# Kernel optimization log

Hardware: AMD Instinct MI355X
Metric: run time of the kernel (lower is better)

Reference implementation:

```python
import jax, jax.numpy as jnp
import numpy as np

EPS = 1e-5  # torch InstanceNorm2d default eps


def _pe_2d(h, w, dim):
    """2D rotary angles: first dim//2 channel-pairs encode row position, rest encode col.
    Returns angles of shape (dim//2, h, w) -- one angle per channel PAIR."""
    half = dim // 2          # channels per axis
    nf = half // 2           # rotation pairs per axis
    inv = 1.0 / (10000.0 ** (jnp.arange(nf, dtype=jnp.float32) * 2.0 / half))
    ang_h = jnp.arange(h, dtype=jnp.float32)[None, :, None] * inv[:, None, None]  # (nf,h,1)
    ang_w = jnp.arange(w, dtype=jnp.float32)[None, None, :] * inv[:, None, None]  # (nf,1,w)
    ang_h = jnp.broadcast_to(ang_h, (nf, h, w))
    ang_w = jnp.broadcast_to(ang_w, (nf, h, w))
    return jnp.concatenate([ang_h, ang_w], axis=0)  # (dim//2, h, w)


def _rope_2d(x, ang):
    """Rotate consecutive channel pairs (2i, 2i+1) of x [b,c,h,w] by angles [c//2,h,w]."""
    b, c, h, w = x.shape
    x1 = x[:, 0::2]  # (b, c//2, h, w)
    x2 = x[:, 1::2]
    cos = jnp.cos(ang)[None]
    sin = jnp.sin(ang)[None]
    r1 = x1 * cos - x2 * sin
    r2 = x1 * sin + x2 * cos
    return jnp.stack([r1, r2], axis=2).reshape(b, c, h, w)


def _conv1x1(t, W, b):
    return jnp.einsum('bchw,oc->bohw', t, W) + b[None, :, None, None]


def setup_inputs() -> dict:
    key = jax.random.key(0)
    ks = jax.random.split(key, 11)
    B, C, H, W, S, O = 16, 256, 64, 64, 128, 256
    f = lambda k, sh: jax.random.normal(k, sh, dtype=jnp.float32)
    return {
        'x': f(ks[0], (B, C, H, W)),
        'gate_W': f(ks[1], (C, C)) * 0.05,  'gate_b': f(ks[2], (C,)) * 0.05,
        'value_W': f(ks[3], (C, C)) * 0.05, 'value_b': f(ks[4], (C,)) * 0.05,
        'z_W': f(ks[5], (S, C)) * 0.05,     'z_b': f(ks[6], (S,)) * 0.05,
        'gamma': jax.random.uniform(ks[7], (2, S), dtype=jnp.float32),
        'beta':  jax.random.uniform(ks[8], (2, S), dtype=jnp.float32),
        'proj_W': f(ks[9], (O, C)) * 0.05,  'proj_b': f(ks[10], (O,)) * 0.05,
    }


def reference(x, gate_W, gate_b, value_W, value_b, z_W, z_b, gamma, beta, proj_W, proj_b):
    b, c, h, w = x.shape
    S = z_W.shape[0]  # scaled_dim
    # InstanceNorm2d (affine=False): normalize each (b,c) plane over h,w (biased var)
    mu = x.mean(axis=(2, 3), keepdims=True)
    var = x.var(axis=(2, 3), keepdims=True)
    x_n = (x - mu) * jax.lax.rsqrt(var + EPS)
    g = _conv1x1(x_n, gate_W, gate_b)
    v = _conv1x1(x_n, value_W, value_b)
    z = _conv1x1(x_n, z_W, z_b)
    # qk = einsum('bchw,pc->bpchw', z, gamma) + beta -> unbind p
    q = z * gamma[0][None, :, None, None] + beta[0][None, :, None, None]
    k = z * gamma[1][None, :, None, None] + beta[1][None, :, None, None]
    ang = _pe_2d(h, w, S)
    q = _rope_2d(q, ang)
    k = _rope_2d(k, ang)
    # per-pixel channel dot product, scaled, then ONE global softmax over h*w per sample
    sim = jnp.einsum('bchw,bchw->bhw', q, k) / jnp.sqrt(jnp.float32(S))
    A = jax.nn.softmax(sim.reshape(b, -1).astype(jnp.float32), axis=-1).reshape(b, h, w)
    # (dropout is identity in eval mode)
    V = A[:, None, :, :] * v * g
    V = V + x_n  # residual=True
    out = _conv1x1(V, proj_W, proj_b)
    return out, A
```

## Files before the change

### kernel.cpp

```cpp
#include <hip/hip_runtime.h>
#include <hip/hip_bf16.h>
#include <cstdint>
#include <cstddef>


typedef __attribute__((ext_vector_type(8))) short short8;
typedef __attribute__((ext_vector_type(4))) float f32x4;
typedef __attribute__((ext_vector_type(2))) float f32x2;
typedef __attribute__((ext_vector_type(4))) unsigned int uint4v;
typedef __attribute__((ext_vector_type(2))) unsigned int uint2v;

#define DI __device__ __forceinline__

DI unsigned int f2bf(float f){ unsigned int i; __builtin_memcpy(&i,&f,4); return (i + 0x7fffu + ((i>>16)&1u))>>16; }
DI float bf2f(unsigned short u){ unsigned int i = ((unsigned int)u)<<16; float f; __builtin_memcpy(&f,&i,4); return f; }
DI unsigned int pk2bf(float lo, float hi){
  float2 f2; f2.x = lo; f2.y = hi;
  __hip_bfloat162 h = __float22bfloat162_rn(f2);
  unsigned int u; __builtin_memcpy(&u, &h, 4); return u;
}

DI void gload16(const void* g, void* l){
  __builtin_amdgcn_global_load_lds((const __attribute__((address_space(1))) void*)g,
                                   (__attribute__((address_space(3))) void*)l, 16, 0, 0);
}

__global__ __launch_bounds__(256) void k_pack_w(
    const float* __restrict__ gW, const float* __restrict__ vW,
    const float* __restrict__ zW, const float* __restrict__ pW,
    const float* __restrict__ gB, const float* __restrict__ vB,
    const float* __restrict__ zB, const float* __restrict__ pB,
    unsigned short* __restrict__ wcat, unsigned short* __restrict__ proj,
    float* __restrict__ biases){
  int id = blockIdx.x*256 + threadIdx.x;
  if (id < 20480){
    int n=id&127, k8=(id>>7)&7, ks=(id>>10)&3, nt=id>>12;
    int o = nt*128+n, c0 = ks*64+k8*8;
    const float* src = (o<256) ? gW + (size_t)o*256 + c0
                      : (o<512) ? vW + (size_t)(o-256)*256 + c0
                      :           zW + (size_t)(o-512)*256 + c0;
    f32x4 a = *(const f32x4*)src, b = *(const f32x4*)(src+4);
    uint4v ov;
    ov[0] = pk2bf(a[0],a[1]); ov[1] = pk2bf(a[2],a[3]);
    ov[2] = pk2bf(b[0],b[1]); ov[3] = pk2bf(b[2],b[3]);
    *(uint4v*)(wcat + (size_t)id*8) = ov;
  } else if (id < 28672){
    int q = id - 20480;
    int m=q&127, k8=(q>>7)&7, ks=(q>>10)&3, mt=q>>12;
    int o = mt*128+m, c0 = ks*64+k8*8;
    const float* src = pW + (size_t)o*256 + c0;
    f32x4 a = *(const f32x4*)src, b = *(const f32x4*)(src+4);
    uint4v ov;
    ov[0] = pk2bf(a[0],a[1]); ov[1] = pk2bf(a[2],a[3]);
    ov[2] = pk2bf(b[0],b[1]); ov[3] = pk2bf(b[2],b[3]);
    *(uint4v*)(proj + (size_t)q*8) = ov;
  }
  if (id < 640) biases[id] = id<256 ? gB[id] : id<512 ? vB[id-256] : zB[id-512];
  if (id < 256) biases[640+id] = pB[id];
}

__global__ __launch_bounds__(256) void k_stats(const float* __restrict__ x, float* __restrict__ stats){
  int bc = blockIdx.x, t = threadIdx.x, lane = t&63, wid = t>>6;
  const f32x4* row = (const f32x4*)(x + (size_t)bc*4096);
  float s=0.f, q=0.f;
  #pragma unroll
  for (int i=0;i<4;i++){
    f32x4 v = row[i*256+t];
    #pragma unroll
    for (int w=0;w<4;w++){ s += v[w]; q += v[w]*v[w]; }
  }
  #pragma unroll
  for (int off=32; off; off>>=1){ s += __shfl_xor(s,off); q += __shfl_xor(q,off); }
  __shared__ float r1[4], r2[4];
  if (lane==0){ r1[wid]=s; r2[wid]=q; }
  __syncthreads();
  if (t==0){
    float S=r1[0]+r1[1]+r1[2]+r1[3], Q=r2[0]+r2[1]+r2[2]+r2[3];
    float mu = S*(1.0f/4096.0f);
    float var = Q*(1.0f/4096.0f) - mu*mu;
    stats[bc*2]   = mu;
    stats[bc*2+1] = rsqrtf(var + 1e-5f);
  }
}

__global__ __launch_bounds__(256) void k_xn_pack(const float* __restrict__ x,
    const float* __restrict__ stats, unsigned short* __restrict__ apack){
  size_t id = (size_t)blockIdx.x*256 + threadIdx.x;
  int m=(int)(id&127), k8=(int)(id>>7)&7, ks=(int)(id>>10)&3, mt=(int)(id>>12)&31, b=(int)(id>>17);
  int hw = mt*128+m, c0 = ks*64+k8*8;
  const float* xp = x + ((size_t)(b*256 + c0))*4096 + hw;
  const float* st = stats + (size_t)(b*256+c0)*2;
  uint4v o;
  #pragma unroll
  for (int j=0;j<8;j+=2){
    float v0 = (xp[(size_t)j*4096]     - st[j*2])   * st[j*2+1];
    float v1 = (xp[(size_t)(j+1)*4096] - st[j*2+2]) * st[j*2+3];
    o[j>>1] = pk2bf(v0, v1);
  }
  *(uint4v*)(apack + id*8) = o;
}

__global__ __launch_bounds__(256,2) void k_gvzf(
    const unsigned short* __restrict__ Ap, const unsigned short* __restrict__ Wc,
    const float* __restrict__ biases, const float* __restrict__ gm, const float* __restrict__ bt,
    unsigned short* __restrict__ gvp, float* __restrict__ sim){
  __shared__ alignas(16) unsigned short lds[2][2][8192];
  __shared__ float red[2][4][16][2];
  int orig = blockIdx.x;
  int wg = (orig&7)*320 + (orig>>3);
  int b = wg/160; int r = wg - b*160; int p = r>>5; int mt = r&31;
  const unsigned short* Xt = Ap + (size_t)(b*32+mt)*32768;
  int t = threadIdx.x, lane = t&63;
  int wo = (t>>6)>>1, wm = (t>>6)&1;

  #define STAGEGV(buf, kss) do{ \
    _Pragma("unroll") \
    for (int i_=0;i_<4;i_++){ \
      int idx_ = i_*256 + t; \
      int k8_ = idx_>>7, slot_ = idx_&127; \
      int half_ = slot_>>6, sl_ = slot_&63; \
      int nt_, n_; \
      if (p<4){ nt_ = (p>>1) + half_*2; n_ = ((p&1)<<6) | sl_; } \
      else    { nt_ = 4; n_ = slot_; } \
      gload16(Wc + ((size_t)(nt_*4+(kss)))*8192 + (size_t)(k8_*128+n_)*8, &lds[buf][0][(size_t)idx_*8]); \
      gload16(Xt + (size_t)(kss)*8192 + (size_t)idx_*8, &lds[buf][1][(size_t)idx_*8]); \
    } \
  }while(0)

  f32x4 accg[2][4]={}, accv[2][4]={};

  #define CGV(buf) do{ \
    _Pragma("unroll") \
    for (int kf_=0;kf_<2;kf_++){ \
      int k8l_ = kf_*4 + (lane>>4); \
      short8 wg_[2], wv_[2], xf_[4]; \
      _Pragma("unroll") for (int ci_=0;ci_<2;ci_++){ \
        int sg_ = wo*32 + ci_*16 + (lane&15); \
        wg_[ci_] = *(const short8*)&lds[buf][0][(size_t)(k8l_*128 + sg_)*8]; \
        wv_[ci_] = *(const short8*)&lds[buf][0][(size_t)(k8l_*128 + 64 + sg_)*8]; } \
      _Pragma("unroll") for (int mj_=0;mj_<4;mj_++) \
        xf_[mj_] = *(const short8*)&lds[buf][1][(size_t)(k8l_*128 + wm*64 + mj_*16 + (lane&15))*8]; \
      _Pragma("unroll") for (int ci_=0;ci_<2;ci_++) \
        _Pragma("unroll") for (int mj_=0;mj_<4;mj_++){ \
          accg[ci_][mj_] = __builtin_amdgcn_mfma_f32_16x16x32_bf16(wg_[ci_], xf_[mj_], accg[ci_][mj_],0,0,0); \
          accv[ci_][mj_] = __builtin_amdgcn_mfma_f32_16x16x32_bf16(wv_[ci_], xf_[mj_], accv[ci_][mj_],0,0,0); } \
    } \
  }while(0)

  STAGEGV(0,0);
  __syncthreads();
  #pragma unroll
  for (int ks=0; ks<4; ++ks){
    int cur = ks&1;
    if (ks<3) STAGEGV(cur^1, ks+1);
    CGV(cur);
    __syncthreads();
  }

  if (p<4){
    #pragma unroll
    for (int ci=0;ci<2;ci++){
      int c = p*64 + wo*32 + ci*16 + ((lane>>4)<<2);
      f32x4 bg = *(const f32x4*)&biases[c];
      f32x4 bv = *(const f32x4*)&biases[256+c];
      int ksO = c>>6, k8O = (c>>3)&7, j0 = c&7;
      size_t base = ((size_t)(b*32+mt)*4 + ksO)*8192 + (size_t)(k8O*128)*8 + j0;
      #pragma unroll
      for (int mj=0;mj<4;mj++){
        int m = wm*64 + mj*16 + (lane&15);
        f32x4 pg = accg[ci][mj] + bg;
        f32x4 pv = accv[ci][mj] + bv;
        uint2v pk;
        pk[0] = pk2bf(pg[0]*pv[0], pg[1]*pv[1]);
        pk[1] = pk2bf(pg[2]*pv[2], pg[3]*pv[3]);
        *(uint2v*)(gvp + base + (size_t)m*8) = pk;
      }
    }
  } else {
    float part[4] = {0.f,0.f,0.f,0.f};
    #pragma unroll
    for (int ci=0;ci<2;ci++){
      int cq = wo*32 + ci*16 + ((lane>>4)<<2);
      f32x4 bz0 = *(const f32x4*)&biases[512+cq];
      f32x4 bz1 = *(const f32x4*)&biases[512+64+cq];
      f32x4 g0a = *(const f32x4*)&gm[cq],      g1a = *(const f32x4*)&gm[128+cq];
      f32x4 b0a = *(const f32x4*)&bt[cq],      b1a = *(const f32x4*)&bt[128+cq];
      f32x4 g0b = *(const f32x4*)&gm[64+cq],   g1b = *(const f32x4*)&gm[192+cq];
      f32x4 b0b = *(const f32x4*)&bt[64+cq],   b1b = *(const f32x4*)&bt[192+cq];
      #pragma unroll
      for (int mj=0;mj<4;mj++){
        f32x4 z0 = accg[ci][mj] + bz0;
        f32x4 z1 = accv[ci][mj] + bz1;
        f32x4 c0 = (z0*g0a + b0a) * (z0*g1a + b1a);
        f32x4 c1 = (z1*g0b + b0b) * (z1*g1b + b1b);
        part[mj] += c0[0]+c0[1]+c0[2]+c0[3] + c1[0]+c1[1]+c1[2]+c1[3];
      }
    }
    #pragma unroll
    for (int mj=0;mj<4;mj++){
      float rr = part[mj];
      rr += __shfl_xor(rr, 16);
      rr += __shfl_xor(rr, 32);
      if (lane < 16) red[wm][mj][lane][wo] = rr;
    }
    __syncthreads();
    if (t < 128){
      int wmq = t>>6, mjq = (t>>4)&3, lq = t&15;
      float s = red[wmq][mjq][lq][0] + red[wmq][mjq][lq][1];
      sim[(size_t)b*4096 + mt*128 + wmq*64 + mjq*16 + lq] = s * 0.08838834764831845f;
    }
  }
  #undef STAGEGV
  #undef CGV
}

__global__ __launch_bounds__(512,1) void k_projf(
    const unsigned short* __restrict__ gvp, const unsigned short* __restrict__ Xp,
    const unsigned short* __restrict__ Wp, const float* __restrict__ biases,
    const float* __restrict__ A, float* __restrict__ out){
  extern __shared__ unsigned short sm[];
  unsigned short* Wl0 = sm;
  unsigned short* Wl1 = sm + 16384;
  unsigned short* Vl0 = sm + 32768;
  unsigned short* Vl1 = sm + 40960;
  int orig = blockIdx.x;
  int wg = (orig&7)*64 + (orig>>3);
  int b = wg>>5, mt = wg&31;
  int t = threadIdx.x, lane = t&63, wid = t>>6;
  int wo = wid>>1, wm = wid&1;
  size_t tbase = (size_t)(b*32+mt)*32768;
  float a = A[(size_t)b*4096 + mt*128 + (t&127)];
  uint4v Gr[2], Xr[2];

  #define LOADV(kss) do{ _Pragma("unroll") for (int i_=0;i_<2;i_++){ \
      Gr[i_] = *(const uint4v*)(gvp + tbase + (size_t)(kss)*8192 + (size_t)(i_*512+t)*8); \
      Xr[i_] = *(const uint4v*)(Xp  + tbase + (size_t)(kss)*8192 + (size_t)(i_*512+t)*8); } }while(0)

  #define WRITEV(DST) do{ _Pragma("unroll") for (int i_=0;i_<2;i_++){ \
      uint4v g_=Gr[i_], x_=Xr[i_]; uint4v o_; \
      _Pragma("unroll") for (int w_=0;w_<4;w_++){ \
        float gA_=bf2f((unsigned short)(g_[w_]&0xffff)), gB_=bf2f((unsigned short)(g_[w_]>>16)); \
        float xA_=bf2f((unsigned short)(x_[w_]&0xffff)), xB_=bf2f((unsigned short)(x_[w_]>>16)); \
        o_[w_] = pk2bf(a*gA_+xA_, a*gB_+xB_); } \
      *(uint4v*)&(DST)[(size_t)(i_*512+t)*8] = o_; } }while(0)

  #define STAGEW(DST, kss) do{ _Pragma("unroll") for (int i_=0;i_<4;i_++){ \
      int idx_ = i_*512+t; \
      int k8_ = idx_>>8, rest_ = idx_&255, oh_ = rest_>>7, o_ = rest_&127; \
      gload16(Wp + (((size_t)(oh_*4+(kss))*8 + k8_)*128 + o_)*8, &(DST)[(size_t)idx_*8]); } }while(0)

  f32x4 acc[4][4]={};

  #define CPJ(WBUF, VBUF) do{ \
    _Pragma("unroll") for (int kf_=0;kf_<2;kf_++){ \
      int k8l_ = kf_*4 + (lane>>4); \
      short8 wf_[4], vf_[4]; \
      _Pragma("unroll") for (int ci_=0;ci_<4;ci_++) \
        wf_[ci_] = *(const short8*)&(WBUF)[(size_t)(k8l_*256 + wo*64 + ci_*16 + (lane&15))*8]; \
      _Pragma("unroll") for (int mj_=0;mj_<4;mj_++) \
        vf_[mj_] = *(const short8*)&(VBUF)[(size_t)(k8l_*128 + wm*64 + mj_*16 + (lane&15))*8]; \
      _Pragma("unroll") for (int ci_=0;ci_<4;ci_++) \
        _Pragma("unroll") for (int mj_=0;mj_<4;mj_++) \
          acc[ci_][mj_] = __builtin_amdgcn_mfma_f32_16x16x32_bf16(wf_[ci_], vf_[mj_], acc[ci_][mj_],0,0,0); \
    } }while(0)

  LOADV(0); STAGEW(Wl0, 0); WRITEV(Vl0);
  __syncthreads();
  LOADV(1); STAGEW(Wl1, 1);
  CPJ(Wl0, Vl0);
  WRITEV(Vl1);
  __syncthreads();
  LOADV(2); STAGEW(Wl0, 2);
  CPJ(Wl1, Vl1);
  WRITEV(Vl0);
  __syncthreads();
  LOADV(3); STAGEW(Wl1, 3);
  CPJ(Wl0, Vl0);
  WRITEV(Vl1);
  __syncthreads();
  CPJ(Wl1, Vl1);
  __syncthreads();

  float* fl = (float*)sm;
  #pragma unroll
  for (int pp=0; pp<2; ++pp){
    if ((wo>>1) == pp){
      #pragma unroll
      for (int ci=0;ci<4;ci++){
        int oq = (wo&1)*64 + ci*16 + ((lane>>4)<<2);
        #pragma unroll
        for (int mj=0;mj<4;mj++){
          int m = wm*64 + mj*16 + (lane&15);
          *(f32x4*)&fl[(size_t)m*128 + (oq ^ (((m>>2)&31)<<2))] = acc[ci][mj];
        }
      }
    }
    __syncthreads();
    #pragma unroll
    for (int it=0; it<8; it++){
      int gid = it*512 + t;
      int o_r = gid>>5, hq = (gid&31)<<2;
      int s = ((hq>>2)&31)<<2;
      float bo = biases[640 + pp*128 + o_r];
      f32x4 vo;
      #pragma unroll
      for (int k=0;k<4;k++) vo[k] = fl[(size_t)(hq+k)*128 + (o_r ^ s)] + bo;
      *(f32x4*)&out[((size_t)(b*256 + pp*128 + o_r))*4096 + mt*128 + hq] = vo;
    }
    __syncthreads();
  }
  #undef LOADV
  #undef WRITEV
  #undef STAGEW
  #undef CPJ
}

__global__ __launch_bounds__(256) void k_softmax(const float* __restrict__ sim, float* __restrict__ A){
  int b = blockIdx.x, t = threadIdx.x, lane = t&63, wid = t>>6;
  const f32x4* s4 = (const f32x4*)(sim + (size_t)b*4096);
  f32x4 v[4];
  float mx = -3.4e38f;
  #pragma unroll
  for (int i=0;i<4;i++){
    v[i] = s4[i*256+t];
    #pragma unroll
    for (int w=0;w<4;w++) mx = fmaxf(mx, v[i][w]);
  }
  #pragma unroll
  for (int off=32; off; off>>=1) mx = fmaxf(mx, __shfl_xor(mx, off));
  __shared__ float sr1[4], sr2[4];
  if (lane==0) sr1[wid]=mx;
  __syncthreads();
  mx = fmaxf(fmaxf(sr1[0],sr1[1]), fmaxf(sr1[2],sr1[3]));
  float sum=0.f;
  #pragma unroll
  for (int i=0;i<4;i++)
    #pragma unroll
    for (int w=0;w<4;w++){ float e = expf(v[i][w]-mx); v[i][w]=e; sum+=e; }
  #pragma unroll
  for (int off=32; off; off>>=1) sum += __shfl_xor(sum, off);
  if (lane==0) sr2[wid]=sum;
  __syncthreads();
  sum = sr2[0]+sr2[1]+sr2[2]+sr2[3];
  float invs = 1.0f/sum;
  f32x4* Ab = (f32x4*)(A + (size_t)b*4096);
  #pragma unroll
  for (int i=0;i<4;i++){
    f32x4 a;
    #pragma unroll
    for (int w=0;w<4;w++) a[w] = v[i][w]*invs;
    Ab[i*256+t] = a;
  }
}

extern "C" void kernel_launch(void* const* d_in, const int* in_sizes, int n_in,
                              void* d_out, int out_size, void* d_ws, size_t ws_size,
                              hipStream_t stream){
  const float* x  = (const float*)d_in[0];
  const float* gW = (const float*)d_in[1];
  const float* gB = (const float*)d_in[2];
  const float* vW = (const float*)d_in[3];
  const float* vB = (const float*)d_in[4];
  const float* zW = (const float*)d_in[5];
  const float* zB = (const float*)d_in[6];
  const float* gm = (const float*)d_in[7];
  const float* bt = (const float*)d_in[8];
  const float* pW = (const float*)d_in[9];
  const float* pB = (const float*)d_in[10];

  char* ws = (char*)d_ws;
  float* stats           = (float*)(ws + 0);
  float* biases          = (float*)(ws + 32768);
  float* sim             = (float*)(ws + 40960);
  unsigned short* wcat   = (unsigned short*)(ws + 303104);
  unsigned short* proj   = (unsigned short*)(ws + 958464);
  unsigned short* apack  = (unsigned short*)(ws + 2097152);
  unsigned short* gvpack = (unsigned short*)(ws + 35651584);

  float* out = (float*)d_out;
  float* A   = out + 16777216;

  hipLaunchKernelGGL(k_pack_w,  dim3(112),  dim3(256), 0, stream, gW, vW, zW, pW, gB, vB, zB, pB, wcat, proj, biases);
  hipLaunchKernelGGL(k_stats,   dim3(4096), dim3(256), 0, stream, x, stats);
  hipLaunchKernelGGL(k_xn_pack, dim3(8192), dim3(256), 0, stream, x, stats, apack);
  hipLaunchKernelGGL(k_gvzf,    dim3(2560), dim3(256), 0, stream, apack, wcat, biases, gm, bt, gvpack, sim);
  hipLaunchKernelGGL(k_softmax, dim3(16),   dim3(256), 0, stream, sim, A);
  hipLaunchKernelGGL(k_projf,   dim3(512),  dim3(512), 98304, stream, gvpack, apack, proj, biases, A, out);
  (void)in_sizes; (void)n_in; (void)out_size; (void)ws_size;
}
```

Baseline: 98.45 us.

## Halve K-chunk size in GEMM kernels to cut LDS and raise occupancy

Both the gate/value/z GEMM and the projection GEMM now stage 32-wide K chunks (8 iterations) instead of 64-wide (4 iterations). This halves their LDS footprint, and the launch bounds are raised so more workgroups can stay resident per CU. The projection epilogue transposes through a smaller 64-column LDS buffer in four passes with an adjusted swizzle. In exchange there are twice as many barriers and pipeline steps, and tighter register limits may cause spills.

```diff
diff --git a/kernel.cpp b/kernel.cpp
--- a/kernel.cpp
+++ b/kernel.cpp
@@ -12,7 +12,6 @@
 
 #define DI __device__ __forceinline__
 
-DI unsigned int f2bf(float f){ unsigned int i; __builtin_memcpy(&i,&f,4); return (i + 0x7fffu + ((i>>16)&1u))>>16; }
 DI float bf2f(unsigned short u){ unsigned int i = ((unsigned int)u)<<16; float f; __builtin_memcpy(&f,&i,4); return f; }
 DI unsigned int pk2bf(float lo, float hi){
   float2 f2; f2.x = lo; f2.y = hi;
@@ -100,11 +99,11 @@
   *(uint4v*)(apack + id*8) = o;
 }
 
-__global__ __launch_bounds__(256,2) void k_gvzf(
+__global__ __launch_bounds__(256,4) void k_gvzf(
     const unsigned short* __restrict__ Ap, const unsigned short* __restrict__ Wc,
     const float* __restrict__ biases, const float* __restrict__ gm, const float* __restrict__ bt,
     unsigned short* __restrict__ gvp, float* __restrict__ sim){
-  __shared__ alignas(16) unsigned short lds[2][2][8192];
+  __shared__ alignas(16) unsigned short lds[2][2][4096];
   __shared__ float red[2][4][16][2];
   int orig = blockIdx.x;
   int wg = (orig&7)*320 + (orig>>3);
@@ -113,46 +112,43 @@
   int t = threadIdx.x, lane = t&63;
   int wo = (t>>6)>>1, wm = (t>>6)&1;
 
-  #define STAGEGV(buf, kss) do{ \
+  #define STAGEGV(buf, cc) do{ \
+    int ks_ = (cc)>>1, k8h_ = ((cc)&1)<<2; \
     _Pragma("unroll") \
-    for (int i_=0;i_<4;i_++){ \
-      int idx_ = i_*256 + t; \
-      int k8_ = idx_>>7, slot_ = idx_&127; \
-      int half_ = slot_>>6, sl_ = slot_&63; \
+    for (int i_=0;i_<2;i_++){ \
+      int u_ = i_*256 + t; \
+      int k8_ = u_>>7, slot_ = u_&127; \
       int nt_, n_; \
-      if (p<4){ nt_ = (p>>1) + half_*2; n_ = ((p&1)<<6) | sl_; } \
+      if (p<4){ nt_ = (p>>1) + (slot_>>6)*2; n_ = ((p&1)<<6) | (slot_&63); } \
       else    { nt_ = 4; n_ = slot_; } \
-      gload16(Wc + ((size_t)(nt_*4+(kss)))*8192 + (size_t)(k8_*128+n_)*8, &lds[buf][0][(size_t)idx_*8]); \
-      gload16(Xt + (size_t)(kss)*8192 + (size_t)idx_*8, &lds[buf][1][(size_t)idx_*8]); \
+      gload16(Wc + ((size_t)(nt_*4+ks_)*8 + k8h_ + k8_)*1024 + (size_t)n_*8, &lds[buf][0][(size_t)u_*8]); \
+      gload16(Xt + ((size_t)((cc)*4 + k8_))*1024 + (size_t)slot_*8, &lds[buf][1][(size_t)u_*8]); \
     } \
   }while(0)
 
   f32x4 accg[2][4]={}, accv[2][4]={};
 
   #define CGV(buf) do{ \
-    _Pragma("unroll") \
-    for (int kf_=0;kf_<2;kf_++){ \
-      int k8l_ = kf_*4 + (lane>>4); \
-      short8 wg_[2], wv_[2], xf_[4]; \
-      _Pragma("unroll") for (int ci_=0;ci_<2;ci_++){ \
-        int sg_ = wo*32 + ci_*16 + (lane&15); \
-        wg_[ci_] = *(const short8*)&lds[buf][0][(size_t)(k8l_*128 + sg_)*8]; \
-        wv_[ci_] = *(const short8*)&lds[buf][0][(size_t)(k8l_*128 + 64 + sg_)*8]; } \
-      _Pragma("unroll") for (int mj_=0;mj_<4;mj_++) \
-        xf_[mj_] = *(const short8*)&lds[buf][1][(size_t)(k8l_*128 + wm*64 + mj_*16 + (lane&15))*8]; \
-      _Pragma("unroll") for (int ci_=0;ci_<2;ci_++) \
-        _Pragma("unroll") for (int mj_=0;mj_<4;mj_++){ \
-          accg[ci_][mj_] = __builtin_amdgcn_mfma_f32_16x16x32_bf16(wg_[ci_], xf_[mj_], accg[ci_][mj_],0,0,0); \
-          accv[ci_][mj_] = __builtin_amdgcn_mfma_f32_16x16x32_bf16(wv_[ci_], xf_[mj_], accv[ci_][mj_],0,0,0); } \
-    } \
+    int k8l_ = lane>>4; \
+    short8 wgf_[2], wvf_[2], xf_[4]; \
+    _Pragma("unroll") for (int ci_=0;ci_<2;ci_++){ \
+      int sg_ = wo*32 + ci_*16 + (lane&15); \
+      wgf_[ci_] = *(const short8*)&lds[buf][0][(size_t)(k8l_*128 + sg_)*8]; \
+      wvf_[ci_] = *(const short8*)&lds[buf][0][(size_t)(k8l_*128 + 64 + sg_)*8]; } \
+    _Pragma("unroll") for (int mj_=0;mj_<4;mj_++) \
+      xf_[mj_] = *(const short8*)&lds[buf][1][(size_t)(k8l_*128 + wm*64 + mj_*16 + (lane&15))*8]; \
+    _Pragma("unroll") for (int ci_=0;ci_<2;ci_++) \
+      _Pragma("unroll") for (int mj_=0;mj_<4;mj_++){ \
+        accg[ci_][mj_] = __builtin_amdgcn_mfma_f32_16x16x32_bf16(wgf_[ci_], xf_[mj_], accg[ci_][mj_],0,0,0); \
+        accv[ci_][mj_] = __builtin_amdgcn_mfma_f32_16x16x32_bf16(wvf_[ci_], xf_[mj_], accv[ci_][mj_],0,0,0); } \
   }while(0)
 
   STAGEGV(0,0);
   __syncthreads();
   #pragma unroll
-  for (int ks=0; ks<4; ++ks){
-    int cur = ks&1;
-    if (ks<3) STAGEGV(cur^1, ks+1);
+  for (int c=0; c<8; ++c){
+    int cur = c&1;
+    if (c<7) STAGEGV(cur^1, c+1);
     CGV(cur);
     __syncthreads();
   }
@@ -214,15 +210,15 @@
   #undef CGV
 }
 
-__global__ __launch_bounds__(512,1) void k_projf(
+__global__ __launch_bounds__(512,4) void k_projf(
     const unsigned short* __restrict__ gvp, const unsigned short* __restrict__ Xp,
     const unsigned short* __restrict__ Wp, const float* __restrict__ biases,
     const float* __restrict__ A, float* __restrict__ out){
   extern __shared__ unsigned short sm[];
   unsigned short* Wl0 = sm;
-  unsigned short* Wl1 = sm + 16384;
-  unsigned short* Vl0 = sm + 32768;
-  unsigned short* Vl1 = sm + 40960;
+  unsigned short* Wl1 = sm + 8192;
+  unsigned short* Vl0 = sm + 16384;
+  unsigned short* Vl1 = sm + 20480;
   int orig = blockIdx.x;
   int wg = (orig&7)*64 + (orig>>3);
   int b = wg>>5, mt = wg&31;
@@ -230,82 +226,82 @@
   int wo = wid>>1, wm = wid&1;
   size_t tbase = (size_t)(b*32+mt)*32768;
   float a = A[(size_t)b*4096 + mt*128 + (t&127)];
-  uint4v Gr[2], Xr[2];
-
-  #define LOADV(kss) do{ _Pragma("unroll") for (int i_=0;i_<2;i_++){ \
-      Gr[i_] = *(const uint4v*)(gvp + tbase + (size_t)(kss)*8192 + (size_t)(i_*512+t)*8); \
-      Xr[i_] = *(const uint4v*)(Xp  + tbase + (size_t)(kss)*8192 + (size_t)(i_*512+t)*8); } }while(0)
-
-  #define WRITEV(DST) do{ _Pragma("unroll") for (int i_=0;i_<2;i_++){ \
-      uint4v g_=Gr[i_], x_=Xr[i_]; uint4v o_; \
+  uint4v Gr, Xr;
+
+  #define LOADV(cc) do{ \
+      size_t off_ = tbase + ((size_t)((cc)*4 + (t>>7)))*1024 + (size_t)(t&127)*8; \
+      Gr = *(const uint4v*)(gvp + off_); \
+      Xr = *(const uint4v*)(Xp  + off_); }while(0)
+
+  #define WRITEV(DST) do{ \
+      uint4v o_; \
       _Pragma("unroll") for (int w_=0;w_<4;w_++){ \
-        float gA_=bf2f((unsigned short)(g_[w_]&0xffff)), gB_=bf2f((unsigned short)(g_[w_]>>16)); \
-        float xA_=bf2f((unsigned short)(x_[w_]&0xffff)), xB_=bf2f((unsigned short)(x_[w_]>>16)); \
+        float gA_=bf2f((unsigned short)(Gr[w_]&0xffff)), gB_=bf2f((unsigned short)(Gr[w_]>>16)); \
+        float xA_=bf2f((unsigned short)(Xr[w_]&0xffff)), xB_=bf2f((unsigned short)(Xr[w_]>>16)); \
         o_[w_] = pk2bf(a*gA_+xA_, a*gB_+xB_); } \
-      *(uint4v*)&(DST)[(size_t)(i_*512+t)*8] = o_; } }while(0)
-
-  #define STAGEW(DST, kss) do{ _Pragma("unroll") for (int i_=0;i_<4;i_++){ \
-      int idx_ = i_*512+t; \
-      int k8_ = idx_>>8, rest_ = idx_&255, oh_ = rest_>>7, o_ = rest_&127; \
-      gload16(Wp + (((size_t)(oh_*4+(kss))*8 + k8_)*128 + o_)*8, &(DST)[(size_t)idx_*8]); } }while(0)
+      *(uint4v*)&(DST)[(size_t)t*8] = o_; }while(0)
+
+  #define STAGEW(DST, cc) do{ \
+    int ks_ = (cc)>>1, k8h_ = ((cc)&1)<<2; \
+    _Pragma("unroll") for (int i_=0;i_<2;i_++){ \
+      int u_ = i_*512 + t; \
+      int k8_ = u_>>8, slot_ = u_&255, oh_ = slot_>>7, o_ = slot_&127; \
+      gload16(Wp + ((size_t)(oh_*4+ks_)*8 + k8h_ + k8_)*1024 + (size_t)o_*8, &(DST)[(size_t)u_*8]); } }while(0)
 
   f32x4 acc[4][4]={};
 
   #define CPJ(WBUF, VBUF) do{ \
-    _Pragma("unroll") for (int kf_=0;kf_<2;kf_++){ \
-      int k8l_ = kf_*4 + (lane>>4); \
-      short8 wf_[4], vf_[4]; \
-      _Pragma("unroll") for (int ci_=0;ci_<4;ci_++) \
-        wf_[ci_] = *(const short8*)&(WBUF)[(size_t)(k8l_*256 + wo*64 + ci_*16 + (lane&15))*8]; \
+    int k8l_ = lane>>4; \
+    short8 wf_[4], vf_[4]; \
+    _Pragma("unroll") for (int ci_=0;ci_<4;ci_++) \
+      wf_[ci_] = *(const short8*)&(WBUF)[(size_t)(k8l_*256 + wo*64 + ci_*16 + (lane&15))*8]; \
+    _Pragma("unroll") for (int mj_=0;mj_<4;mj_++) \
+      vf_[mj_] = *(const short8*)&(VBUF)[(size_t)(k8l_*128 + wm*64 + mj_*16 + (lane&15))*8]; \
+    _Pragma("unroll") for (int ci_=0;ci_<4;ci_++) \
       _Pragma("unroll") for (int mj_=0;mj_<4;mj_++) \
-        vf_[mj_] = *(const short8*)&(VBUF)[(size_t)(k8l_*128 + wm*64 + mj_*16 + (lane&15))*8]; \
-      _Pragma("unroll") for (int ci_=0;ci_<4;ci_++) \
-        _Pragma("unroll") for (int mj_=0;mj_<4;mj_++) \
-          acc[ci_][mj_] = __builtin_amdgcn_mfma_f32_16x16x32_bf16(wf_[ci_], vf_[mj_], acc[ci_][mj_],0,0,0); \
-    } }while(0)
+        acc[ci_][mj_] = __builtin_amdgcn_mfma_f32_16x16x32_bf16(wf_[ci_], vf_[mj_], acc[ci_][mj_],0,0,0); \
+  }while(0)
 
   LOADV(0); STAGEW(Wl0, 0); WRITEV(Vl0);
   __syncthreads();
-  LOADV(1); STAGEW(Wl1, 1);
-  CPJ(Wl0, Vl0);
-  WRITEV(Vl1);
-  __syncthreads();
-  LOADV(2); STAGEW(Wl0, 2);
-  CPJ(Wl1, Vl1);
-  WRITEV(Vl0);
-  __syncthreads();
-  LOADV(3); STAGEW(Wl1, 3);
-  CPJ(Wl0, Vl0);
-  WRITEV(Vl1);
-  __syncthreads();
-  CPJ(Wl1, Vl1);
-  __syncthreads();
+  #pragma unroll
+  for (int c=0; c<8; ++c){
+    if (c<7){
+      LOADV(c+1);
+      if (c&1) STAGEW(Wl0, c+1); else STAGEW(Wl1, c+1);
+    }
+    if (c&1) CPJ(Wl1, Vl1); else CPJ(Wl0, Vl0);
+    if (c<7){ if (c&1) WRITEV(Vl0); else WRITEV(Vl1); }
+    __syncthreads();
+  }
 
   float* fl = (float*)sm;
   #pragma unroll
-  for (int pp=0; pp<2; ++pp){
-    if ((wo>>1) == pp){
+  for (int pp=0; pp<4; ++pp){
+    if (wo == pp){
       #pragma unroll
       for (int ci=0;ci<4;ci++){
-        int oq = (wo&1)*64 + ci*16 + ((lane>>4)<<2);
+        int oq = ci*16 + ((lane>>4)<<2);
         #pragma unroll
         for (int mj=0;mj<4;mj++){
           int m = wm*64 + mj*16 + (lane&15);
-          *(f32x4*)&fl[(size_t)m*128 + (oq ^ (((m>>2)&31)<<2))] = acc[ci][mj];
+          *(f32x4*)&fl[(size_t)m*64 + (oq ^ (((m>>2)&15)<<2))] = acc[ci][mj];
         }
       }
     }
     __syncthreads();
     #pragma unroll
-    for (int it=0; it<8; it++){
+    for (int it=0; it<4; it++){
       int gid = it*512 + t;
       int o_r = gid>>5, hq = (gid&31)<<2;
-      int s = ((hq>>2)&31)<<2;
-      float bo = biases[640 + pp*128 + o_r];
+      float bo = biases[640 + pp*64 + o_r];
       f32x4 vo;
       #pragma unroll
-      for (int k=0;k<4;k++) vo[k] = fl[(size_t)(hq+k)*128 + (o_r ^ s)] + bo;
-      *(f32x4*)&out[((size_t)(b*256 + pp*128 + o_r))*4096 + mt*128 + hq] = vo;
+      for (int k=0;k<4;k++){
+        int m2 = hq+k;
+        vo[k] = fl[(size_t)m2*64 + (o_r ^ (((m2>>2)&15)<<2))] + bo;
+      }
+      *(f32x4*)&out[((size_t)(b*256 + pp*64 + o_r))*4096 + mt*128 + hq] = vo;
     }
     __syncthreads();
   }
@@ -385,6 +381,6 @@
   hipLaunchKernelGGL(k_xn_pack, dim3(8192), dim3(256), 0, stream, x, stats, apack);
   hipLaunchKernelGGL(k_gvzf,    dim3(2560), dim3(256), 0, stream, apack, wcat, biases, gm, bt, gvpack, sim);
   hipLaunchKernelGGL(k_softmax, dim3(16),   dim3(256), 0, stream, sim, A);
-  hipLaunchKernelGGL(k_projf,   dim3(512),  dim3(512), 98304, stream, gvpack, apack, proj, biases, A, out);
+  hipLaunchKernelGGL(k_projf,   dim3(512),  dim3(512), 49152, stream, gvpack, apack, proj, biases, A, out);
   (void)in_sizes; (void)n_in; (void)out_size; (void)ws_size;
 }
```

Result: slower. 111.5 us (+13.3%).
